# Performance work log

Measured on AMD Instinct MI355X. Metric: run time of the kernel, lower is better.

Reference implementation:

```python
import jax, jax.numpy as jnp
import numpy as np

N_NODES = 200000
N_EDGES = 3200000
N_FEAT = 602
N_CLASS = 41


def setup_inputs() -> dict:
    key = jax.random.key(0)
    k1, k2, k3 = jax.random.split(key, 3)
    x = jax.random.normal(k1, (N_NODES, N_FEAT), dtype=jnp.float32)
    W = jax.random.normal(k2, (N_FEAT, N_CLASS), dtype=jnp.float32) * (1.0 / np.sqrt(N_FEAT))
    b = jnp.zeros((N_CLASS,), dtype=jnp.float32)
    edge_index = jax.random.randint(k3, (2, N_EDGES), 0, N_NODES, dtype=jnp.int64)
    return {"x": x, "W": W, "b": b, "edge_index": edge_index}


def reference(x, W, b, edge_index):
    # GCNConv: add self-loops, symmetric normalization, linear transform,
    # scatter-add aggregation, bias; then log_softmax (module forward).
    N = x.shape[0]
    loops = jnp.arange(N, dtype=edge_index.dtype)
    src = jnp.concatenate([edge_index[0], loops])  # [E+N]
    dst = jnp.concatenate([edge_index[1], loops])  # [E+N]
    # degree of A + I computed on destination index
    deg = jax.ops.segment_sum(jnp.ones(src.shape, dtype=x.dtype), dst, num_segments=N)
    dinv = jax.lax.rsqrt(jnp.maximum(deg, 1.0))  # deg >= 1 due to self-loops
    norm = dinv[src] * dinv[dst]                 # [E+N]
    h = x @ W                                    # [N, C] transform before aggregation (C < F)
    msg = h[src] * norm[:, None]                 # [E+N, C]
    agg = jax.ops.segment_sum(msg, dst, num_segments=N) + b  # [N, C]
    z = jax.nn.log_softmax(agg, axis=1)
    return (agg, z)
```

## Files before the change

### kernel.cpp

```cpp
#include <hip/hip_runtime.h>
#include <hip/hip_bf16.h>
#include <math.h>

#define F 602
#define C 41
#define HP_STRIDE 48
#define KSTEPS 19
#define GROWS 64
#define ASTRIDE 616

typedef short short8 __attribute__((ext_vector_type(8)));
typedef float f32x4 __attribute__((ext_vector_type(4)));

static __device__ __forceinline__ unsigned short f2bf(float f){
  unsigned int x = __float_as_uint(f);
  x += 0x7FFFu + ((x >> 16) & 1u);
  return (unsigned short)(x >> 16);
}
static __device__ __forceinline__ float bf2f(unsigned short u){
  return __uint_as_float(((unsigned int)u) << 16);
}

__global__ void k_flag(const int* __restrict__ e32, int* __restrict__ flag){
  __shared__ int s[256];
  int t = threadIdx.x;
  int v = 0;
  for (int i = t; i < 2048; i += 256) v |= e32[2*i + 1];
  s[t] = v; __syncthreads();
  for (int off = 128; off > 0; off >>= 1){
    if (t < off) s[t] |= s[t + off];
    __syncthreads();
  }
  if (t == 0) flag[0] = (s[0] == 0) ? 1 : 0;
}

static __device__ __forceinline__ int eidx(const int* __restrict__ p, int is64, long long pos){
  return is64 ? p[2*pos] : p[pos];
}

__global__ void k_count(const int* __restrict__ ei, const int* __restrict__ flag,
                        int* __restrict__ count, int E){
  int e = blockIdx.x * 256 + threadIdx.x;
  if (e >= E) return;
  int is64 = flag[0];
  int d = eidx(ei, is64, (long long)E + e);
  atomicAdd(&count[d], 1);
}

__global__ void k_scan1(const int* __restrict__ count, int* __restrict__ rs,
                        float* __restrict__ dinv, int* __restrict__ bsum, int N){
  __shared__ int s[256];
  int t = threadIdx.x;
  int base = blockIdx.x * 2048 + t * 8;
  int v[8]; int tot = 0;
  #pragma unroll
  for (int j = 0; j < 8; j++){
    int i = base + j;
    int c = (i < N) ? count[i] : 0;
    v[j] = c; tot += c;
    if (i < N) dinv[i] = rsqrtf((float)(c + 1));
  }
  s[t] = tot; __syncthreads();
  for (int off = 1; off < 256; off <<= 1){
    int x = (t >= off) ? s[t - off] : 0;
    __syncthreads();
    s[t] += x;
    __syncthreads();
  }
  int run = s[t] - tot;
  #pragma unroll
  for (int j = 0; j < 8; j++){
    int i = base + j;
    if (i < N) rs[i] = run;
    run += v[j];
  }
  if (t == 255) bsum[blockIdx.x] = s[255];
}

__global__ void k_scan2(int* __restrict__ bsum, int nb){
  __shared__ int s[256];
  int t = threadIdx.x;
  int v = (t < nb) ? bsum[t] : 0;
  s[t] = v; __syncthreads();
  for (int off = 1; off < 256; off <<= 1){
    int x = (t >= off) ? s[t - off] : 0;
    __syncthreads();
    s[t] += x;
    __syncthreads();
  }
  if (t < nb) bsum[t] = s[t] - v;
}

__global__ void k_scan3(int* __restrict__ rs, int* __restrict__ cur,
                        const int* __restrict__ bsum, int N, int E){
  int i = blockIdx.x * 256 + threadIdx.x;
  if (i == 0) rs[N] = E;
  if (i >= N) return;
  int r = rs[i] + bsum[i >> 11];
  rs[i] = r; cur[i] = r;
}

__global__ void k_fill(const int* __restrict__ ei, const int* __restrict__ flag,
                       int* __restrict__ cur, int* __restrict__ csr, int E){
  int e = blockIdx.x * 256 + threadIdx.x;
  if (e >= E) return;
  int is64 = flag[0];
  int s = eidx(ei, is64, e);
  int d = eidx(ei, is64, (long long)E + e);
  int pos = atomicAdd(&cur[d], 1);
  csr[pos] = s;
}

__global__ void k_wprep(const float* __restrict__ W, unsigned short* __restrict__ Wf){
  int idx = blockIdx.x * 256 + threadIdx.x;
  if (idx >= KSTEPS * 3 * 64) return;
  int lane = idx & 63;
  int nt = (idx >> 6) % 3;
  int s = idx / (3 * 64);
  int quad = lane >> 4, l16 = lane & 15;
  int n = nt * 16 + l16;
  unsigned int w[4];
  #pragma unroll
  for (int p = 0; p < 4; p++){
    int k0 = s * 32 + quad * 8 + 2 * p;
    float lo = (k0     < F && n < C) ? W[k0 * C + n]       : 0.f;
    float hi = (k0 + 1 < F && n < C) ? W[(k0 + 1) * C + n] : 0.f;
    w[p] = (unsigned)f2bf(lo) | ((unsigned)f2bf(hi) << 16);
  }
  ((uint4*)Wf)[idx] = make_uint4(w[0], w[1], w[2], w[3]);
}

__global__ __launch_bounds__(256) void k_gemm3(const float* __restrict__ x,
        const unsigned short* __restrict__ Wf, unsigned short* __restrict__ hp, int N){
  __shared__ unsigned short As[GROWS * ASTRIDE];
  const int t = threadIdx.x;
  const long long rb0 = (long long)blockIdx.x * GROWS;
  for (int i = t; i < GROWS * 6; i += 256){
    int r = i / 6, c = 602 + (i - r * 6);
    As[r * ASTRIDE + c] = 0;
  }
  long long nrow = (long long)N - rb0; if (nrow > GROWS) nrow = GROWS;
  const int limit = (int)(nrow * F);
  const float* base = x + rb0 * F;
  #pragma unroll 4
  for (int f4 = t; f4 * 4 < limit; f4 += 256){
    int idx = f4 * 4;
    float4 v = *(const float4*)(base + idx);
    int row = idx / F;
    int col = idx - row * F;
    if (col <= F - 4){
      int a = row * ASTRIDE + col;
      unsigned p0 = (unsigned)f2bf(v.x) | ((unsigned)f2bf(v.y) << 16);
      unsigned p1 = (unsigned)f2bf(v.z) | ((unsigned)f2bf(v.w) << 16);
      *(unsigned*)&As[a]     = p0;
      *(unsigned*)&As[a + 2] = p1;
    } else {
      float e[4] = {v.x, v.y, v.z, v.w};
      #pragma unroll
      for (int q = 0; q < 4; q++){
        int ii = idx + q;
        int r2 = ii / F, c2 = ii - r2 * F;
        As[r2 * ASTRIDE + c2] = f2bf(e[q]);
      }
    }
  }
  __syncthreads();
  const int wv = t >> 6, lane = t & 63;
  const int quad = lane >> 4, l16 = lane & 15;
  const unsigned short* arow = &As[(wv * 16 + l16) * ASTRIDE + quad * 8];
  const short8* wf8 = (const short8*)Wf;
  f32x4 acc0 = {0.f,0.f,0.f,0.f}, acc1 = acc0, acc2 = acc0;
  #pragma unroll
  for (int s = 0; s < KSTEPS; s++){
    short8 a  = *(const short8*)(arow + s * 32);
    short8 b0 = wf8[(s * 3 + 0) * 64 + lane];
    short8 b1 = wf8[(s * 3 + 1) * 64 + lane];
    short8 b2 = wf8[(s * 3 + 2) * 64 + lane];
    acc0 = __builtin_amdgcn_mfma_f32_16x16x32_bf16(a, b0, acc0, 0, 0, 0);
    acc1 = __builtin_amdgcn_mfma_f32_16x16x32_bf16(a, b1, acc1, 0, 0, 0);
    acc2 = __builtin_amdgcn_mfma_f32_16x16x32_bf16(a, b2, acc2, 0, 0, 0);
  }
  int rl = wv * 16 + quad * 4;
  #pragma unroll
  for (int reg = 0; reg < 4; reg++){
    long long grow = rb0 + rl + reg;
    if (grow < N){
      unsigned short* hr = hp + grow * HP_STRIDE;
      hr[0 * 16 + l16] = f2bf(acc0[reg]);
      hr[1 * 16 + l16] = f2bf(acc1[reg]);
      hr[2 * 16 + l16] = f2bf(acc2[reg]);
    }
  }
}

__global__ __launch_bounds__(256) void k_agg(const unsigned short* __restrict__ hp,
        const int* __restrict__ csr, const int* __restrict__ rs,
        const float* __restrict__ dinv, const float* __restrict__ b,
        float* __restrict__ agg, int N){
  int node = blockIdx.x * 4 + (threadIdx.x >> 6);
  int lane = threadIdx.x & 63;
  if (node >= N) return;
  int beg = rs[node], end = rs[node + 1];
  float dn = dinv[node];
  bool act = lane < C;
  float acc = 0.f;
  if (act) acc = dn * dn * bf2f(hp[(long long)node * HP_STRIDE + lane]);
  int i = beg;
  for (; i + 3 < end; i += 4){
    int s0 = csr[i], s1 = csr[i+1], s2 = csr[i+2], s3 = csr[i+3];
    float n0 = dinv[s0] * dn, n1 = dinv[s1] * dn;
    float n2 = dinv[s2] * dn, n3 = dinv[s3] * dn;
    float h0 = 0.f, h1 = 0.f, h2 = 0.f, h3 = 0.f;
    if (act){
      h0 = bf2f(hp[(long long)s0 * HP_STRIDE + lane]);
      h1 = bf2f(hp[(long long)s1 * HP_STRIDE + lane]);
      h2 = bf2f(hp[(long long)s2 * HP_STRIDE + lane]);
      h3 = bf2f(hp[(long long)s3 * HP_STRIDE + lane]);
    }
    acc = fmaf(n0, h0, acc); acc = fmaf(n1, h1, acc);
    acc = fmaf(n2, h2, acc); acc = fmaf(n3, h3, acc);
  }
  for (; i < end; i++){
    int s0 = csr[i];
    float n0 = dinv[s0] * dn;
    if (act) acc = fmaf(n0, bf2f(hp[(long long)s0 * HP_STRIDE + lane]), acc);
  }
  if (act) agg[(long long)node * C + lane] = acc + b[lane];
}

__global__ __launch_bounds__(256) void k_lsm(const float* __restrict__ agg,
        float* __restrict__ z, int N){
  int node = blockIdx.x * 4 + (threadIdx.x >> 6);
  int lane = threadIdx.x & 63;
  if (node >= N) return;
  bool act = lane < C;
  float a = act ? agg[(long long)node * C + lane] : -3.0e38f;
  float m = a;
  #pragma unroll
  for (int off = 32; off > 0; off >>= 1) m = fmaxf(m, __shfl_xor(m, off, 64));
  float ex = act ? expf(a - m) : 0.f;
  float s = ex;
  #pragma unroll
  for (int off = 32; off > 0; off >>= 1) s += __shfl_xor(s, off, 64);
  if (act) z[(long long)node * C + lane] = a - m - logf(s);
}

extern "C" void kernel_launch(void* const* d_in, const int* in_sizes, int n_in,
                              void* d_out, int out_size, void* d_ws, size_t ws_size,
                              hipStream_t stream){
  const float* x = (const float*)d_in[0];
  const float* W = (const float*)d_in[1];
  const float* b = (const float*)d_in[2];
  const int*   ei = (const int*)d_in[3];
  int N = in_sizes[0] / F;
  int E = in_sizes[3] / 2;

  float* out = (float*)d_out;
  float* agg = out;
  float* z   = out + (long long)N * C;
  unsigned short* hp = (unsigned short*)z;

  char* ws = (char*)d_ws;
  auto al = [](size_t v){ return (v + 255) & ~size_t(255); };
  size_t o = 0;
  int*   flag  = (int*)(ws + o);  o = al(o + 4);
  int*   count = (int*)(ws + o);  o = al(o + (size_t)N * 4);
  float* dinv  = (float*)(ws + o); o = al(o + (size_t)N * 4);
  int*   rs    = (int*)(ws + o);  o = al(o + ((size_t)N + 1) * 4);
  int*   cur   = (int*)(ws + o);  o = al(o + (size_t)N * 4);
  int*   bsum  = (int*)(ws + o);  o = al(o + 4096);
  unsigned short* Wf = (unsigned short*)(ws + o); o = al(o + (size_t)KSTEPS * 3 * 64 * 16);
  int*   csr   = (int*)(ws + o);  o = al(o + (size_t)E * 4);

  int nb_e    = (E + 255) / 256;
  int nb_scan = (N + 2047) / 2048;
  int nb_n    = (N + 255) / 256;
  int nb_g    = (N + GROWS - 1) / GROWS;
  int nb_node = (N + 3) / 4;
  int nb_w    = (KSTEPS * 3 * 64 + 255) / 256;

  k_flag<<<1, 256, 0, stream>>>(ei, flag);
  hipMemsetAsync(count, 0, (size_t)N * 4, stream);
  k_count<<<nb_e, 256, 0, stream>>>(ei, flag, count, E);
  k_wprep<<<nb_w, 256, 0, stream>>>(W, Wf);
  k_scan1<<<nb_scan, 256, 0, stream>>>(count, rs, dinv, bsum, N);
  k_scan2<<<1, 256, 0, stream>>>(bsum, nb_scan);
  k_scan3<<<nb_n, 256, 0, stream>>>(rs, cur, bsum, N, E);
  k_fill<<<nb_e, 256, 0, stream>>>(ei, flag, cur, csr, E);
  k_gemm3<<<nb_g, 256, 0, stream>>>(x, Wf, hp, N);
  k_agg<<<nb_node, 256, 0, stream>>>(hp, csr, rs, dinv, b, agg, N);
  k_lsm<<<nb_node, 256, 0, stream>>>(agg, z, N);
}
```

Baseline: 1.298 ms.

## Fuse log_softmax into aggregation, move h buffer to workspace, unroll gather by 8

Merges the log_softmax kernel into the aggregation kernel, so the aggregated row stays in registers and is not read back from memory. Because the z output is now written during aggregation, the bf16 transformed features move from the z output region to a dedicated workspace buffer, and the row stride grows to 64 so the address becomes a shift and rows align to 128 bytes. The gather loop adds an 8-way unrolled stage to keep more loads in flight. The cost is a larger h buffer, which means more GEMM write bytes, and higher register pressure.

```diff
diff --git a/kernel.cpp b/kernel.cpp
--- a/kernel.cpp
+++ b/kernel.cpp
@@ -4,7 +4,7 @@
 
 #define F 602
 #define C 41
-#define HP_STRIDE 48
+#define HP_STRIDE 64
 #define KSTEPS 19
 #define GROWS 64
 #define ASTRIDE 616
@@ -196,26 +196,51 @@
 __global__ __launch_bounds__(256) void k_agg(const unsigned short* __restrict__ hp,
         const int* __restrict__ csr, const int* __restrict__ rs,
         const float* __restrict__ dinv, const float* __restrict__ b,
-        float* __restrict__ agg, int N){
+        float* __restrict__ agg, float* __restrict__ z, int N){
   int node = blockIdx.x * 4 + (threadIdx.x >> 6);
   int lane = threadIdx.x & 63;
   if (node >= N) return;
   int beg = rs[node], end = rs[node + 1];
   float dn = dinv[node];
   bool act = lane < C;
+  const unsigned short* hb = hp + lane;
   float acc = 0.f;
-  if (act) acc = dn * dn * bf2f(hp[(long long)node * HP_STRIDE + lane]);
+  if (act) acc = dn * dn * bf2f(hb[(long long)node << 6]);
   int i = beg;
+  for (; i + 7 < end; i += 8){
+    int s0 = csr[i],   s1 = csr[i+1], s2 = csr[i+2], s3 = csr[i+3];
+    int s4 = csr[i+4], s5 = csr[i+5], s6 = csr[i+6], s7 = csr[i+7];
+    float n0 = dinv[s0] * dn, n1 = dinv[s1] * dn;
+    float n2 = dinv[s2] * dn, n3 = dinv[s3] * dn;
+    float n4 = dinv[s4] * dn, n5 = dinv[s5] * dn;
+    float n6 = dinv[s6] * dn, n7 = dinv[s7] * dn;
+    float h0 = 0.f, h1 = 0.f, h2 = 0.f, h3 = 0.f;
+    float h4 = 0.f, h5 = 0.f, h6 = 0.f, h7 = 0.f;
+    if (act){
+      h0 = bf2f(hb[(long long)s0 << 6]);
+      h1 = bf2f(hb[(long long)s1 << 6]);
+      h2 = bf2f(hb[(long long)s2 << 6]);
+      h3 = bf2f(hb[(long long)s3 << 6]);
+      h4 = bf2f(hb[(long long)s4 << 6]);
+      h5 = bf2f(hb[(long long)s5 << 6]);
+      h6 = bf2f(hb[(long long)s6 << 6]);
+      h7 = bf2f(hb[(long long)s7 << 6]);
+    }
+    acc = fmaf(n0, h0, acc); acc = fmaf(n1, h1, acc);
+    acc = fmaf(n2, h2, acc); acc = fmaf(n3, h3, acc);
+    acc = fmaf(n4, h4, acc); acc = fmaf(n5, h5, acc);
+    acc = fmaf(n6, h6, acc); acc = fmaf(n7, h7, acc);
+  }
   for (; i + 3 < end; i += 4){
     int s0 = csr[i], s1 = csr[i+1], s2 = csr[i+2], s3 = csr[i+3];
     float n0 = dinv[s0] * dn, n1 = dinv[s1] * dn;
     float n2 = dinv[s2] * dn, n3 = dinv[s3] * dn;
     float h0 = 0.f, h1 = 0.f, h2 = 0.f, h3 = 0.f;
     if (act){
-      h0 = bf2f(hp[(long long)s0 * HP_STRIDE + lane]);
-      h1 = bf2f(hp[(long long)s1 * HP_STRIDE + lane]);
-      h2 = bf2f(hp[(long long)s2 * HP_STRIDE + lane]);
-      h3 = bf2f(hp[(long long)s3 * HP_STRIDE + lane]);
+      h0 = bf2f(hb[(long long)s0 << 6]);
+      h1 = bf2f(hb[(long long)s1 << 6]);
+      h2 = bf2f(hb[(long long)s2 << 6]);
+      h3 = bf2f(hb[(long long)s3 << 6]);
     }
     acc = fmaf(n0, h0, acc); acc = fmaf(n1, h1, acc);
     acc = fmaf(n2, h2, acc); acc = fmaf(n3, h3, acc);
@@ -223,18 +248,13 @@
   for (; i < end; i++){
     int s0 = csr[i];
     float n0 = dinv[s0] * dn;
-    if (act) acc = fmaf(n0, bf2f(hp[(long long)s0 * HP_STRIDE + lane]), acc);
-  }
-  if (act) agg[(long long)node * C + lane] = acc + b[lane];
-}
-
-__global__ __launch_bounds__(256) void k_lsm(const float* __restrict__ agg,
-        float* __restrict__ z, int N){
-  int node = blockIdx.x * 4 + (threadIdx.x >> 6);
-  int lane = threadIdx.x & 63;
-  if (node >= N) return;
-  bool act = lane < C;
-  float a = act ? agg[(long long)node * C + lane] : -3.0e38f;
+    if (act) acc = fmaf(n0, bf2f(hb[(long long)s0 << 6]), acc);
+  }
+  float a = -3.0e38f;
+  if (act){
+    a = acc + b[lane];
+    agg[(long long)node * C + lane] = a;
+  }
   float m = a;
   #pragma unroll
   for (int off = 32; off > 0; off >>= 1) m = fmaxf(m, __shfl_xor(m, off, 64));
@@ -258,7 +278,6 @@
   float* out = (float*)d_out;
   float* agg = out;
   float* z   = out + (long long)N * C;
-  unsigned short* hp = (unsigned short*)z;
 
   char* ws = (char*)d_ws;
   auto al = [](size_t v){ return (v + 255) & ~size_t(255); };
@@ -271,6 +290,7 @@
   int*   bsum  = (int*)(ws + o);  o = al(o + 4096);
   unsigned short* Wf = (unsigned short*)(ws + o); o = al(o + (size_t)KSTEPS * 3 * 64 * 16);
   int*   csr   = (int*)(ws + o);  o = al(o + (size_t)E * 4);
+  unsigned short* hp = (unsigned short*)(ws + o); o = al(o + (size_t)N * HP_STRIDE * 2);
 
   int nb_e    = (E + 255) / 256;
   int nb_scan = (N + 2047) / 2048;
@@ -288,6 +308,5 @@
   k_scan3<<<nb_n, 256, 0, stream>>>(rs, cur, bsum, N, E);
   k_fill<<<nb_e, 256, 0, stream>>>(ei, flag, cur, csr, E);
   k_gemm3<<<nb_g, 256, 0, stream>>>(x, Wf, hp, N);
-  k_agg<<<nb_node, 256, 0, stream>>>(hp, csr, rs, dinv, b, agg, N);
-  k_lsm<<<nb_node, 256, 0, stream>>>(agg, z, N);
-}
+  k_agg<<<nb_node, 256, 0, stream>>>(hp, csr, rs, dinv, b, agg, z, N);
+}
```

Result: no change. 1.276 ms (-1.6%).
